# Kernel optimization log

Hardware: AMD Instinct MI355X
Metric: run time of the kernel (lower is better)

The kernel has to match this reference:

```python
import jax, jax.numpy as jnp
import numpy as np

B, T, H, DQK, DV = 2, 8192, 8, 128, 128
HID = H * DQK  # 1024
CHUNK = 64
EPS = 1e-5


def hedgehog(x, w, b):
    # torch Linear: y = x @ W.T + b, then softmax over cat([2y, -2y])
    y = x @ w.T + b
    return jax.nn.softmax(jnp.concatenate([2.0 * y, -2.0 * y], axis=-1), axis=-1)


def rmsnorm(x):
    return x * jax.lax.rsqrt(jnp.mean(x * x, axis=-1, keepdims=True) + EPS)


def chunk_linear_attn(q, k, v):
    # q, k: [B, T, H, Dk]; v: [B, T, H, Dv]  (head_first=False)
    scale = q.shape[-1] ** -0.5
    q = q * scale
    Bq, Tq, Hq, Dk = q.shape
    Dv = v.shape[-1]
    nc = Tq // CHUNK

    def to_chunks(t):
        # [B, T, H, D] -> [nc, B, H, C, D]
        return t.reshape(Bq, nc, CHUNK, Hq, -1).transpose(1, 0, 3, 2, 4)

    qc, kc, vc = to_chunks(q), to_chunks(k), to_chunks(v)
    mask = jnp.tril(jnp.ones((CHUNK, CHUNK), dtype=bool))

    def step(S, qkv):
        qi, ki, vi = qkv  # [B, H, C, D]
        attn = jnp.einsum('bhcd,bhed->bhce', qi, ki)      # intra-chunk scores
        attn = jnp.where(mask, attn, 0.0)                 # causal within chunk
        o = jnp.einsum('bhce,bhev->bhcv', attn, vi) \
            + jnp.einsum('bhcd,bhdv->bhcv', qi, S)        # inter-chunk via state
        S = S + jnp.einsum('bhcd,bhcv->bhdv', ki, vi)
        return S, o

    S0 = jnp.zeros((Bq, Hq, Dk, Dv), q.dtype)
    _, oc = jax.lax.scan(step, S0, (qc, kc, vc))          # oc: [nc, B, H, C, Dv]
    return oc.transpose(1, 0, 3, 2, 4).reshape(Bq, Tq, Hq, Dv)


def setup_inputs() -> dict:
    key = jax.random.key(0)
    ks = jax.random.split(key, 9)
    gain = 2.0 ** (-2.5)

    def xavier(k, shape):
        bound = gain * np.sqrt(6.0 / (shape[0] + shape[1]))
        return jax.random.uniform(k, shape, jnp.float32, -bound, bound)

    return {
        'x': jax.random.normal(ks[0], (B, T, HID), jnp.float32),
        'Wq': xavier(ks[1], (HID, HID)),
        'Wk': xavier(ks[2], (HID, HID)),
        'Wv': xavier(ks[3], (HID, HID)),
        'Wo': xavier(ks[4], (HID, HID)),
        # self.apply xavier-inits the hedgehog Linear layers too (no _is_hf_initialized flag)
        'fmq_w': xavier(ks[5], (DQK, DQK)),
        'fmq_b': jnp.zeros((DQK,), jnp.float32),
        'fmk_w': xavier(ks[6], (DQK, DQK)),
        'fmk_b': jnp.zeros((DQK,), jnp.float32),
    }


def reference(x, Wq, Wk, Wv, Wo, fmq_w, fmq_b, fmk_w, fmk_b):
    q = (x @ Wq.T).reshape(B, T, H, DQK)
    k = (x @ Wk.T).reshape(B, T, H, DQK)
    v = (x @ Wv.T).reshape(B, T, H, DV)
    q = hedgehog(q, fmq_w, fmq_b)   # [B, T, H, 2*DQK]
    k = hedgehog(k, fmk_w, fmk_b)   # [B, T, H, 2*DQK]
    o = chunk_linear_attn(q, k, v)  # [B, T, H, DV]
    o = rmsnorm(o.reshape(B, T, H * DV))
    return o @ Wo.T
```

## Files before the change

### kernel.cpp

```cpp
#include <hip/hip_runtime.h>
#include <stdint.h>

typedef unsigned short u16;
typedef __bf16 bf16x8 __attribute__((ext_vector_type(8)));
typedef float f32x4 __attribute__((ext_vector_type(4)));
typedef float f32x16 __attribute__((ext_vector_type(16)));

__device__ __forceinline__ u16 f2b(float f) {
  union { float f; unsigned u; } v; v.f = f;
  unsigned r = v.u + 0x7fffu + ((v.u >> 16) & 1u);
  return (u16)(r >> 16);
}
__device__ __forceinline__ float b2f(u16 b) {
  union { unsigned u; float f; } v; v.u = ((unsigned)b) << 16;
  return v.f;
}

__device__ __forceinline__ int swz64(int b) {
  return b ^ (((((b >> 6) & 3) ^ ((b >> 8) & 1))) << 4);
}

__global__ __launch_bounds__(256) void cast_bf16(const float* __restrict__ in,
                                                 u16* __restrict__ out, int n4) {
  int i = blockIdx.x * 256 + threadIdx.x;
  if (i >= n4) return;
  float4 f = ((const float4*)in)[i];
  ushort4 r = make_ushort4(f2b(f.x), f2b(f.y), f2b(f.z), f2b(f.w));
  ((ushort4*)out)[i] = r;
}

__global__ __launch_bounds__(256) void fold_w(const float* __restrict__ W,
                                              const float* __restrict__ fmw,
                                              u16* __restrict__ out) {
  int hj = blockIdx.x;
  int h = hj >> 7, j = hj & 127;
  int i0 = threadIdx.x * 4;
  float a0 = 0.f, a1 = 0.f, a2 = 0.f, a3 = 0.f;
  const float* Wh = W + (size_t)(h * 128) * 1024 + i0;
  const float* fw = fmw + j * 128;
  for (int d = 0; d < 128; ++d) {
    float wv = fw[d];
    const float* wr = Wh + (size_t)d * 1024;
    a0 += wv * wr[0]; a1 += wv * wr[1]; a2 += wv * wr[2]; a3 += wv * wr[3];
  }
  ushort4 r = make_ushort4(f2b(a0), f2b(a1), f2b(a2), f2b(a3));
  ((ushort4*)(out + (size_t)hj * 1024))[threadIdx.x] = r;
}

__global__ __launch_bounds__(512, 2) void gemm256(const u16* __restrict__ A,
                                                  const u16* __restrict__ B,
                                                  u16* __restrict__ C,
                                                  int M, int N, int K, int LNT) {
  __shared__ u16 lds[65536];
  const int tid = threadIdx.x, w = tid >> 6, lane = tid & 63;
  int g = blockIdx.x;
  int wg = (g & 7) * ((int)gridDim.x >> 3) + (g >> 3);
  const int nt = wg & ((1 << LNT) - 1), mt = wg >> LNT;
  const int m0 = mt << 8, n0 = nt << 8;
  const int wm = w >> 2, wn = w & 3;
  const int fm = lane & 15, fkb = (lane >> 4) << 4;

  int so0 = w * 1024 + lane * 16;
  int so1 = so0 + 8192;
  const int p0s = swz64(so0), p1s = swz64(so1);
  const size_t ga0 = (size_t)(p0s >> 6) * K + ((p0s & 63) >> 1);
  const size_t ga1 = (size_t)(p1s >> 6) * K + ((p1s & 63) >> 1);
  so0 >>= 1; so1 >>= 1;
#define STAGE(g0, slot)                                                               \
  do {                                                                                \
    __builtin_amdgcn_global_load_lds(                                                 \
        (const __attribute__((address_space(1))) unsigned int*)((g0) + ga0),          \
        (__attribute__((address_space(3))) unsigned int*)((slot) + so0), 16, 0, 0);   \
    __builtin_amdgcn_global_load_lds(                                                 \
        (const __attribute__((address_space(1))) unsigned int*)((g0) + ga1),          \
        (__attribute__((address_space(3))) unsigned int*)((slot) + so1), 16, 0, 0);   \
  } while (0)

  int aoff[2][4], boff[4];
#pragma unroll
  for (int mh = 0; mh < 2; ++mh)
#pragma unroll
    for (int mi = 0; mi < 4; ++mi)
      aoff[mh][mi] = swz64((wm * 128 + mh * 64 + mi * 16 + fm) * 64 + fkb) >> 1;
#pragma unroll
  for (int ni = 0; ni < 4; ++ni)
    boff[ni] = swz64((wn * 64 + ni * 16 + fm) * 64 + fkb) >> 1;

  const u16* Ag = A + (size_t)m0 * K;
  const u16* Bg = B + (size_t)n0 * K;
  const int NT = K >> 6;
  f32x4 acc[8][4] = {};

  STAGE(Ag, lds);
  STAGE(Bg, lds + 32768);
  STAGE(Ag + 32, lds + 8192);
  STAGE(Bg + 32, lds + 32768 + 8192);
  STAGE(Ag + 64, lds + 16384);
  STAGE(Bg + 64, lds + 32768 + 16384);
  asm volatile("s_waitcnt vmcnt(4)" ::: "memory");
  __builtin_amdgcn_s_barrier();

  for (int t = 0; t < NT; ++t) {
    const int buf = t & 1, nb = buf ^ 1;
    const u16* As0 = lds + buf * 16384;
    const u16* As1 = As0 + 8192;
    const u16* Bs0 = lds + 32768 + buf * 16384;
    const u16* Bs1 = Bs0 + 8192;
    bf16x8 a[4], bfr[4];

#pragma unroll
    for (int mi = 0; mi < 4; ++mi) a[mi] = *(const bf16x8*)(As0 + aoff[0][mi]);
#pragma unroll
    for (int ni = 0; ni < 4; ++ni) bfr[ni] = *(const bf16x8*)(Bs0 + boff[ni]);
    if (t + 1 < NT) STAGE(Ag + (t + 1) * 64 + 32, lds + nb * 16384 + 8192);
    __builtin_amdgcn_s_barrier();
    asm volatile("s_waitcnt lgkmcnt(0)" ::: "memory");
    __builtin_amdgcn_sched_barrier(0);
    __builtin_amdgcn_s_setprio(1);
#pragma unroll
    for (int mi = 0; mi < 4; ++mi)
#pragma unroll
      for (int ni = 0; ni < 4; ++ni)
        acc[mi][ni] = __builtin_amdgcn_mfma_f32_16x16x32_bf16(a[mi], bfr[ni], acc[mi][ni], 0, 0, 0);
    __builtin_amdgcn_s_setprio(0);
    __builtin_amdgcn_s_barrier();

#pragma unroll
    for (int mi = 0; mi < 4; ++mi) a[mi] = *(const bf16x8*)(As0 + aoff[1][mi]);
    if (t + 1 < NT) STAGE(Bg + (t + 1) * 64 + 32, lds + 32768 + nb * 16384 + 8192);
    __builtin_amdgcn_s_barrier();
    asm volatile("s_waitcnt lgkmcnt(0)" ::: "memory");
    __builtin_amdgcn_sched_barrier(0);
    __builtin_amdgcn_s_setprio(1);
#pragma unroll
    for (int mi = 0; mi < 4; ++mi)
#pragma unroll
      for (int ni = 0; ni < 4; ++ni)
        acc[4 + mi][ni] =
            __builtin_amdgcn_mfma_f32_16x16x32_bf16(a[mi], bfr[ni], acc[4 + mi][ni], 0, 0, 0);
    __builtin_amdgcn_s_setprio(0);
    __builtin_amdgcn_s_barrier();

#pragma unroll
    for (int mi = 0; mi < 4; ++mi) a[mi] = *(const bf16x8*)(As1 + aoff[0][mi]);
#pragma unroll
    for (int ni = 0; ni < 4; ++ni) bfr[ni] = *(const bf16x8*)(Bs1 + boff[ni]);
    if (t + 2 < NT) STAGE(Ag + (t + 2) * 64, lds + buf * 16384);
    __builtin_amdgcn_s_barrier();
    asm volatile("s_waitcnt lgkmcnt(0)" ::: "memory");
    __builtin_amdgcn_sched_barrier(0);
    __builtin_amdgcn_s_setprio(1);
#pragma unroll
    for (int mi = 0; mi < 4; ++mi)
#pragma unroll
      for (int ni = 0; ni < 4; ++ni)
        acc[mi][ni] = __builtin_amdgcn_mfma_f32_16x16x32_bf16(a[mi], bfr[ni], acc[mi][ni], 0, 0, 0);
    __builtin_amdgcn_s_setprio(0);
    __builtin_amdgcn_s_barrier();

#pragma unroll
    for (int mi = 0; mi < 4; ++mi) a[mi] = *(const bf16x8*)(As1 + aoff[1][mi]);
    if (t + 2 < NT) STAGE(Bg + (t + 2) * 64, lds + 32768 + buf * 16384);
    __builtin_amdgcn_s_barrier();
    asm volatile("s_waitcnt lgkmcnt(0)" ::: "memory");
    __builtin_amdgcn_sched_barrier(0);
    __builtin_amdgcn_s_setprio(1);
#pragma unroll
    for (int mi = 0; mi < 4; ++mi)
#pragma unroll
      for (int ni = 0; ni < 4; ++ni)
        acc[4 + mi][ni] =
            __builtin_amdgcn_mfma_f32_16x16x32_bf16(a[mi], bfr[ni], acc[4 + mi][ni], 0, 0, 0);
    __builtin_amdgcn_s_setprio(0);
    if (t < NT - 2)
      asm volatile("s_waitcnt vmcnt(4)" ::: "memory");
    else
      asm volatile("s_waitcnt vmcnt(0)" ::: "memory");
    __builtin_amdgcn_s_barrier();
  }
#undef STAGE

  u16* Cs = lds;
  const int cr = (lane >> 4) << 2, cc = lane & 15;
#pragma unroll
  for (int am = 0; am < 8; ++am)
#pragma unroll
    for (int ni = 0; ni < 4; ++ni)
#pragma unroll
      for (int r = 0; r < 4; ++r)
        Cs[(wm * 128 + (am >> 2) * 64 + (am & 3) * 16 + cr + r) * 256 + wn * 64 + ni * 16 + cc] =
            f2b(acc[am][ni][r]);
  __syncthreads();
#pragma unroll
  for (int pass = 0; pass < 16; ++pass) {
    int row = pass * 16 + (tid >> 5);
    int colb = (tid & 31) << 4;
    *(uint4*)((char*)(C + (size_t)(m0 + row) * N + n0) + colb) =
        *(const uint4*)((const char*)(Cs + row * 256) + colb);
  }
}

template <int OUT_BF16>
__global__ __launch_bounds__(256) void gemm_bt(const u16* __restrict__ A,
                                               const u16* __restrict__ B,
                                               void* __restrict__ Cv,
                                               int M, int N, int K, int SWZ, int LNT) {
  __shared__ u16 smem[16384];
  u16* As = smem;
  u16* Bs = smem + 8192;
  const int tid = threadIdx.x;
  int g = blockIdx.y * gridDim.x + blockIdx.x;
  int xcd = g & 7, local = g >> 3;
  int mt, nt;
  if (SWZ == 0) {
    mt = xcd * ((int)gridDim.y >> 3) + (local >> LNT);
    nt = local & ((1 << LNT) - 1);
  } else {
    nt = xcd * ((int)gridDim.x >> 3) + (local >> 3);
    mt = local & 7;
  }
  const int m0 = mt * 128, n0 = nt * 128;
  const int wave = tid >> 6, lane = tid & 63;
  const int wm = (wave >> 1) << 6, wn = (wave & 1) << 6;
  f32x4 acc[4][4] = {};
  const int srow = tid >> 3;
  const int scol = (tid & 7) << 3;
  const u16* Ab = A + (size_t)(m0 + srow) * K + scol;
  const u16* Bb = B + (size_t)(n0 + srow) * K + scol;
  u16* Asp = As + srow * 64 + scol;
  u16* Bsp = Bs + srow * 64 + scol;
  const int fm = lane & 15;
  const int fk = (lane >> 4) << 3;
  for (int kt = 0; kt < K; kt += 64) {
#pragma unroll
    for (int i = 0; i < 4; ++i) {
      __builtin_amdgcn_global_load_lds(
          (__attribute__((address_space(1))) unsigned int*)(Ab + (size_t)i * 32 * K + kt),
          (__attribute__((address_space(3))) unsigned int*)(Asp + i * 32 * 64), 16, 0, 0);
      __builtin_amdgcn_global_load_lds(
          (__attribute__((address_space(1))) unsigned int*)(Bb + (size_t)i * 32 * K + kt),
          (__attribute__((address_space(3))) unsigned int*)(Bsp + i * 32 * 64), 16, 0, 0);
    }
    __syncthreads();
#pragma unroll
    for (int kb = 0; kb < 2; ++kb) {
      bf16x8 af[4], bfr[4];
#pragma unroll
      for (int i = 0; i < 4; ++i)
        af[i] = *(const bf16x8*)(As + (wm + i * 16 + fm) * 64 + kb * 32 + fk);
#pragma unroll
      for (int j = 0; j < 4; ++j)
        bfr[j] = *(const bf16x8*)(Bs + (wn + j * 16 + fm) * 64 + kb * 32 + fk);
#pragma unroll
      for (int i = 0; i < 4; ++i)
#pragma unroll
        for (int j = 0; j < 4; ++j)
          acc[i][j] = __builtin_amdgcn_mfma_f32_16x16x32_bf16(af[i], bfr[j], acc[i][j], 0, 0, 0);
    }
    __syncthreads();
  }
  const int cr = (lane >> 4) << 2;
  const int cc = lane & 15;
  if (OUT_BF16) {
    u16* Cs = smem;
#pragma unroll
    for (int i = 0; i < 4; ++i)
#pragma unroll
      for (int j = 0; j < 4; ++j)
#pragma unroll
        for (int r = 0; r < 4; ++r)
          Cs[(wm + i * 16 + cr + r) * 128 + wn + j * 16 + cc] = f2b(acc[i][j][r]);
    __syncthreads();
    u16* Cg = (u16*)Cv;
#pragma unroll
    for (int i = 0; i < 8; ++i) {
      int row = (i >> 1) * 32 + (tid >> 3);
      int col = ((i & 1) * 8 + (tid & 7)) * 8;
      *(uint4*)(Cg + (size_t)(m0 + row) * N + n0 + col) = *(const uint4*)(Cs + row * 128 + col);
    }
  } else {
    float* Csf = (float*)smem;
    float* Cg = (float*)Cv;
#pragma unroll
    for (int hh = 0; hh < 2; ++hh) {
      __syncthreads();
      if ((wm >> 6) == hh) {
#pragma unroll
        for (int i = 0; i < 4; ++i)
#pragma unroll
          for (int j = 0; j < 4; ++j)
#pragma unroll
            for (int r = 0; r < 4; ++r)
              Csf[(i * 16 + cr + r) * 128 + wn + j * 16 + cc] = acc[i][j][r];
      }
      __syncthreads();
#pragma unroll
      for (int i = 0; i < 8; ++i) {
        int row = (i >> 1) * 16 + (tid >> 4);
        int col = ((i & 1) * 16 + (tid & 15)) * 4;
        *(float4*)(Cg + (size_t)(m0 + hh * 64 + row) * N + n0 + col) =
            *(const float4*)(Csf + row * 128 + col);
      }
    }
  }
}

__global__ __launch_bounds__(256) void hedgehog_sm(const u16* __restrict__ y,
                                                   const float* __restrict__ bias,
                                                   u16* __restrict__ phi, float scale,
                                                   int colbase) {
  int wave = threadIdx.x >> 6, lane = threadIdx.x & 63;
  int rh = blockIdx.x * 4 + wave;
  const u16* yr = y + (size_t)(rh >> 3) * 2048 + colbase + (rh & 7) * 128;
  float a1 = 2.f * (b2f(yr[lane]) + bias[lane]);
  float a2 = 2.f * (b2f(yr[lane + 64]) + bias[lane + 64]);
  float mx = fmaxf(fabsf(a1), fabsf(a2));
#pragma unroll
  for (int off = 32; off; off >>= 1) mx = fmaxf(mx, __shfl_xor(mx, off, 64));
  float e1 = __expf(a1 - mx), e2 = __expf(a2 - mx);
  float n1 = __expf(-a1 - mx), n2 = __expf(-a2 - mx);
  float s = e1 + e2 + n1 + n2;
#pragma unroll
  for (int off = 32; off; off >>= 1) s += __shfl_xor(s, off, 64);
  float inv = scale / s;
  u16* pr = phi + (size_t)rh * 256;
  pr[lane] = f2b(e1 * inv);
  pr[lane + 64] = f2b(e2 * inv);
  pr[lane + 128] = f2b(n1 * inv);
  pr[lane + 192] = f2b(n2 * inv);
}

__global__ __launch_bounds__(256, 1) void attn_intra_kv2(const u16* __restrict__ phi_q,
                                                         const u16* __restrict__ phi_k,
                                                         const u16* __restrict__ vt,
                                                         float* __restrict__ o,
                                                         u16* __restrict__ kv) {
  __shared__ u16 lds[18432];
  u16* At = lds;
  u16* Kt = lds;
  int g = blockIdx.x;
  int n = g & 63, h = g >> 6;
  int t0 = n * 128;
  const u16* qg = phi_q + ((size_t)t0 * 8 + h) * 256;
  const u16* kg = phi_k + ((size_t)t0 * 8 + h) * 256;
  const u16* vg = vt + (size_t)(h * 128) * 8192 + t0;
  int tid = threadIdx.x, lane = tid & 63, w = tid >> 6;
  const int fr = lane & 31, fg = (lane >> 5) << 3;
  const int rbase = (lane >> 5) << 2;
  const int mw = (w >> 1) << 6;
  const int nw = (w & 1) << 6;

  f32x16 accS[2][2] = {};
#pragma unroll
  for (int ks = 0; ks < 16; ++ks) {
    bf16x8 a[2], b[2];
#pragma unroll
    for (int i = 0; i < 2; ++i)
      a[i] = *(const bf16x8*)(qg + (size_t)(mw + i * 32 + fr) * 2048 + ks * 16 + fg);
#pragma unroll
    for (int j = 0; j < 2; ++j)
      b[j] = *(const bf16x8*)(kg + (size_t)(nw + j * 32 + fr) * 2048 + ks * 16 + fg);
#pragma unroll
    for (int i = 0; i < 2; ++i)
#pragma unroll
      for (int j = 0; j < 2; ++j)
        accS[i][j] = __builtin_amdgcn_mfma_f32_32x32x16_bf16(a[i], b[j], accS[i][j], 0, 0, 0);
  }
#pragma unroll
  for (int i = 0; i < 2; ++i)
#pragma unroll
    for (int j = 0; j < 2; ++j) {
      int col = nw + j * 32 + (lane & 31);
#pragma unroll
      for (int r = 0; r < 16; ++r) {
        int row = mw + i * 32 + (r & 3) + ((r >> 2) << 3) + rbase;
        At[row * 136 + col] = f2b(col <= row ? accS[i][j][r] : 0.f);
      }
    }
  __syncthreads();
  f32x16 accO[2][2] = {};
#pragma unroll
  for (int ks = 0; ks < 8; ++ks) {
    bf16x8 a[2], b[2];
#pragma unroll
    for (int i = 0; i < 2; ++i)
      a[i] = *(const bf16x8*)(At + (mw + i * 32 + fr) * 136 + ks * 16 + fg);
#pragma unroll
    for (int j = 0; j < 2; ++j)
      b[j] = *(const bf16x8*)(vg + (size_t)(nw + j * 32 + fr) * 8192 + ks * 16 + fg);
#pragma unroll
    for (int i = 0; i < 2; ++i)
#pragma unroll
      for (int j = 0; j < 2; ++j)
        accO[i][j] = __builtin_amdgcn_mfma_f32_32x32x16_bf16(a[i], b[j], accO[i][j], 0, 0, 0);
  }
  {
    float* og = o + ((size_t)t0 * 8 + h) * 128;
#pragma unroll
    for (int i = 0; i < 2; ++i)
#pragma unroll
      for (int j = 0; j < 2; ++j) {
        int vc = nw + j * 32 + (lane & 31);
#pragma unroll
        for (int r = 0; r < 16; ++r) {
          int row = mw + i * 32 + (r & 3) + ((r >> 2) << 3) + rbase;
          og[(size_t)row * 1024 + vc] = accO[i][j][r];
        }
      }
  }
  __syncthreads();

  const int nd = w << 6;
  f32x16 accKV[4][2] = {};
#pragma unroll
  for (int hb = 0; hb < 2; ++hb) {
    {
      int r4 = (tid & 15) << 2;
      int d0 = (tid >> 4) << 4;
      u16 tmp[4][16];
#pragma unroll
      for (int r = 0; r < 4; ++r) {
        const u16* src = kg + (size_t)(hb * 64 + r4 + r) * 2048 + d0;
        *(uint4*)(tmp[r]) = *(const uint4*)src;
        *(uint4*)(tmp[r] + 8) = *(const uint4*)(src + 8);
      }
#pragma unroll
      for (int jj = 0; jj < 16; ++jj) {
        ushort4 pk = make_ushort4(tmp[0][jj], tmp[1][jj], tmp[2][jj], tmp[3][jj]);
        *(ushort4*)(Kt + (d0 + jj) * 72 + r4) = pk;
      }
    }
    __syncthreads();
#pragma unroll
    for (int ks = 0; ks < 4; ++ks) {
      bf16x8 a[4], b[2];
#pragma unroll
      for (int mi = 0; mi < 4; ++mi)
        a[mi] = *(const bf16x8*)(vg + (size_t)(mi * 32 + fr) * 8192 + hb * 64 + ks * 16 + fg);
#pragma unroll
      for (int nj = 0; nj < 2; ++nj)
        b[nj] = *(const bf16x8*)(Kt + (nd + nj * 32 + fr) * 72 + ks * 16 + fg);
#pragma unroll
      for (int mi = 0; mi < 4; ++mi)
#pragma unroll
        for (int nj = 0; nj < 2; ++nj)
          accKV[mi][nj] =
              __builtin_amdgcn_mfma_f32_32x32x16_bf16(a[mi], b[nj], accKV[mi][nj], 0, 0, 0);
    }
    __syncthreads();
  }
  {
    u16* kvg = kv + (size_t)g * 32768;
#pragma unroll
    for (int mi = 0; mi < 4; ++mi)
#pragma unroll
      for (int nj = 0; nj < 2; ++nj) {
        f32x16 acc = accKV[mi][nj];
        int d = nd + nj * 32 + (lane & 31);
#pragma unroll
        for (int r = 0; r < 16; ++r) {
          int vc = mi * 32 + (r & 3) + ((r >> 2) << 3) + rbase;
          kvg[(size_t)vc * 256 + d] = f2b(acc[r]);
        }
      }
  }
}

__global__ __launch_bounds__(256) void kv_scan2(u16* __restrict__ kv) {
  int idx = blockIdx.x * 256 + threadIdx.x;
  int h = idx >> 13;
  int e4 = idx & 8191;
  u16* p = kv + (size_t)h * 2097152 + (size_t)e4 * 4;
  float run[4] = {};
  for (int nn = 0; nn < 64; ++nn) {
    uint2 raw = *(const uint2*)p;
    u16* rv = (u16*)&raw;
    uint2 outw;
    u16* ov = (u16*)&outw;
#pragma unroll
    for (int i = 0; i < 4; ++i) {
      float v = b2f(rv[i]);
      ov[i] = f2b(run[i]);
      run[i] += v;
    }
    *(uint2*)p = outw;
    p += 32768;
  }
}

__global__ __launch_bounds__(256, 1) void attn_inter2(const u16* __restrict__ phi_q,
                                                      const u16* __restrict__ kv,
                                                      float* __restrict__ o) {
  int g = blockIdx.x;
  int n = g & 63, h = g >> 6;
  int t0 = n * 128;
  const u16* qg = phi_q + ((size_t)t0 * 8 + h) * 256;
  const u16* sg = kv + (size_t)g * 32768;
  int tid = threadIdx.x, lane = tid & 63, w = tid >> 6;
  const int fr = lane & 31, fg = (lane >> 5) << 3;
  const int rbase = (lane >> 5) << 2;
  const int mw = (w >> 1) << 6;
  const int nw = (w & 1) << 6;
  f32x16 acc[2][2] = {};
#pragma unroll
  for (int ks = 0; ks < 16; ++ks) {
    bf16x8 a[2], b[2];
#pragma unroll
    for (int i = 0; i < 2; ++i)
      a[i] = *(const bf16x8*)(qg + (size_t)(mw + i * 32 + fr) * 2048 + ks * 16 + fg);
#pragma unroll
    for (int j = 0; j < 2; ++j)
      b[j] = *(const bf16x8*)(sg + (size_t)(nw + j * 32 + fr) * 256 + ks * 16 + fg);
#pragma unroll
    for (int i = 0; i < 2; ++i)
#pragma unroll
      for (int j = 0; j < 2; ++j)
        acc[i][j] = __builtin_amdgcn_mfma_f32_32x32x16_bf16(a[i], b[j], acc[i][j], 0, 0, 0);
  }
  float* og = o + ((size_t)t0 * 8 + h) * 128;
#pragma unroll
  for (int i = 0; i < 2; ++i)
#pragma unroll
    for (int j = 0; j < 2; ++j) {
      int vc = nw + j * 32 + (lane & 31);
#pragma unroll
      for (int r = 0; r < 16; ++r) {
        int row = mw + i * 32 + (r & 3) + ((r >> 2) << 3) + rbase;
        og[(size_t)row * 1024 + vc] += acc[i][j][r];
      }
    }
}

__global__ __launch_bounds__(256) void rmsnorm_k(const float* __restrict__ o,
                                                 u16* __restrict__ on) {
  __shared__ float red[4];
  int row = blockIdx.x;
  const float* orow = o + (size_t)row * 1024;
  int tid = threadIdx.x;
  float4 v = ((const float4*)orow)[tid];
  float ss = v.x * v.x + v.y * v.y + v.z * v.z + v.w * v.w;
#pragma unroll
  for (int off = 32; off; off >>= 1) ss += __shfl_xor(ss, off, 64);
  if ((tid & 63) == 0) red[tid >> 6] = ss;
  __syncthreads();
  float tot = red[0] + red[1] + red[2] + red[3];
  float rms = rsqrtf(tot * (1.f / 1024.f) + 1e-5f);
  ushort4 r = make_ushort4(f2b(v.x * rms), f2b(v.y * rms), f2b(v.z * rms), f2b(v.w * rms));
  ((ushort4*)(on + (size_t)row * 1024))[tid] = r;
}

extern "C" void kernel_launch(void* const* d_in, const int* in_sizes, int n_in,
                              void* d_out, int out_size, void* d_ws, size_t ws_size,
                              hipStream_t stream) {
  const float* x     = (const float*)d_in[0];
  const float* Wq    = (const float*)d_in[1];
  const float* Wk    = (const float*)d_in[2];
  const float* Wv    = (const float*)d_in[3];
  const float* Wo    = (const float*)d_in[4];
  const float* fmq_w = (const float*)d_in[5];
  const float* fmq_b = (const float*)d_in[6];
  const float* fmk_w = (const float*)d_in[7];
  const float* fmk_b = (const float*)d_in[8];

  char* ws = (char*)d_ws;
  u16*   kvb  = (u16*)(ws + 0);
  u16*   xb   = (u16*)(ws + 0);
  u16*   yb   = (u16*)(ws + 16777216);
  u16*   onb  = (u16*)(ws + 50331648);
  u16*   phiq = (u16*)(ws + 67108864);
  u16*   phik = (u16*)(ws + 100663296);
  u16*   vtb  = (u16*)(ws + 134217728);
  float* obuf = (float*)(ws + 150994944);
  u16*   wqkc = (u16*)(ws + 184549376);
  u16*   wvb  = (u16*)(ws + 188743680);
  u16*   wob  = (u16*)(ws + 190840832);

  cast_bf16<<<1024, 256, 0, stream>>>(Wv, wvb, 262144);
  cast_bf16<<<1024, 256, 0, stream>>>(Wo, wob, 262144);
  fold_w<<<1024, 256, 0, stream>>>(Wq, fmq_w, wqkc);
  fold_w<<<1024, 256, 0, stream>>>(Wk, fmk_w, wqkc + 1048576);

  for (int b = 0; b < 2; ++b) {
    const float* xsrc = x + (size_t)b * 8388608;
    float* osrc = (float*)d_out + (size_t)b * 8388608;
    cast_bf16<<<8192, 256, 0, stream>>>(xsrc, xb, 2097152);
    gemm256<<<256, 512, 0, stream>>>(xb, wqkc, yb, 8192, 2048, 1024, 3);
    hedgehog_sm<<<16384, 256, 0, stream>>>(yb, fmq_b, phiq, 0.0625f, 0);
    hedgehog_sm<<<16384, 256, 0, stream>>>(yb, fmk_b, phik, 1.0f, 1024);
    gemm_bt<1><<<dim3(64, 8), 256, 0, stream>>>(wvb, xb, vtb, 1024, 8192, 1024, 1, 0);
    attn_intra_kv2<<<512, 256, 0, stream>>>(phiq, phik, vtb, obuf, kvb);
    kv_scan2<<<256, 256, 0, stream>>>(kvb);
    attn_inter2<<<512, 256, 0, stream>>>(phiq, kvb, obuf);
    rmsnorm_k<<<8192, 256, 0, stream>>>(obuf, onb);
    gemm_bt<0><<<dim3(8, 64), 256, 0, stream>>>(onb, wob, osrc, 8192, 1024, 1024, 0, 3);
  }
}
```

Before: 666.2 us.

## Stage K, Q and V tiles in swizzled LDS via async global-to-LDS loads in attention kernel

The intra-chunk attention kernel now copies the whole phi_k tile, the V^T tile and each half of phi_q into 128 KB of LDS using global_load_lds, with an XOR swizzle. The QK^T, AV and K^T V MFMA loops then read operands from LDS instead of issuing strided global loads directly into registers. The A and K-transpose scratch buffers are re-laid out with swizzles in place of padding, and __syncthreads is replaced by explicit waitcnt plus barrier. This is meant to cut redundant global traffic and uncoalesced loads, at the cost of far more LDS per block and forcing one block per CU.

After: 642.1 us. -3.6%, faster.

```diff
diff --git a/kernel.cpp b/kernel.cpp
--- a/kernel.cpp
+++ b/kernel.cpp
@@ -19,6 +19,8 @@
 __device__ __forceinline__ int swz64(int b) {
   return b ^ (((((b >> 6) & 3) ^ ((b >> 8) & 1))) << 4);
 }
+
+#define SB0() __builtin_amdgcn_sched_barrier(0)
 
 __global__ __launch_bounds__(256) void cast_bf16(const float* __restrict__ in,
                                                  u16* __restrict__ out, int n4) {
@@ -115,7 +117,7 @@
     if (t + 1 < NT) STAGE(Ag + (t + 1) * 64 + 32, lds + nb * 16384 + 8192);
     __builtin_amdgcn_s_barrier();
     asm volatile("s_waitcnt lgkmcnt(0)" ::: "memory");
-    __builtin_amdgcn_sched_barrier(0);
+    SB0();
     __builtin_amdgcn_s_setprio(1);
 #pragma unroll
     for (int mi = 0; mi < 4; ++mi)
@@ -130,7 +132,7 @@
     if (t + 1 < NT) STAGE(Bg + (t + 1) * 64 + 32, lds + 32768 + nb * 16384 + 8192);
     __builtin_amdgcn_s_barrier();
     asm volatile("s_waitcnt lgkmcnt(0)" ::: "memory");
-    __builtin_amdgcn_sched_barrier(0);
+    SB0();
     __builtin_amdgcn_s_setprio(1);
 #pragma unroll
     for (int mi = 0; mi < 4; ++mi)
@@ -148,7 +150,7 @@
     if (t + 2 < NT) STAGE(Ag + (t + 2) * 64, lds + buf * 16384);
     __builtin_amdgcn_s_barrier();
     asm volatile("s_waitcnt lgkmcnt(0)" ::: "memory");
-    __builtin_amdgcn_sched_barrier(0);
+    SB0();
     __builtin_amdgcn_s_setprio(1);
 #pragma unroll
     for (int mi = 0; mi < 4; ++mi)
@@ -163,7 +165,7 @@
     if (t + 2 < NT) STAGE(Bg + (t + 2) * 64, lds + 32768 + buf * 16384);
     __builtin_amdgcn_s_barrier();
     asm volatile("s_waitcnt lgkmcnt(0)" ::: "memory");
-    __builtin_amdgcn_sched_barrier(0);
+    SB0();
     __builtin_amdgcn_s_setprio(1);
 #pragma unroll
     for (int mi = 0; mi < 4; ++mi)
@@ -330,14 +332,17 @@
   pr[lane + 192] = f2b(n2 * inv);
 }
 
-__global__ __launch_bounds__(256, 1) void attn_intra_kv2(const u16* __restrict__ phi_q,
-                                                         const u16* __restrict__ phi_k,
-                                                         const u16* __restrict__ vt,
-                                                         float* __restrict__ o,
-                                                         u16* __restrict__ kv) {
-  __shared__ u16 lds[18432];
-  u16* At = lds;
-  u16* Kt = lds;
+__global__ __launch_bounds__(256, 1) void attn_fused(const u16* __restrict__ phi_q,
+                                                     const u16* __restrict__ phi_k,
+                                                     const u16* __restrict__ vt,
+                                                     float* __restrict__ o,
+                                                     u16* __restrict__ kv) {
+  __shared__ u16 lds[65536];
+  u16* Ks = lds;
+  u16* Vs = lds + 32768;
+  u16* Qh = lds + 49152;
+  u16* At = lds + 49152;
+  u16* Kt = lds + 49152;
   int g = blockIdx.x;
   int n = g & 63, h = g >> 6;
   int t0 = n * 128;
@@ -350,22 +355,78 @@
   const int mw = (w >> 1) << 6;
   const int nw = (w & 1) << 6;
 
+  const int c8 = (tid & 31) << 3;
+  const int rkq = tid >> 5;
+  const int cv = (tid & 15) << 3;
+  const int rv = tid >> 4;
+#pragma unroll
+  for (int i = 0; i < 16; ++i) {
+    int row = i * 8 + rkq;
+    int cs = c8 ^ ((row & 15) << 3);
+    __builtin_amdgcn_global_load_lds(
+        (const __attribute__((address_space(1))) unsigned int*)(kg + (size_t)row * 2048 + cs),
+        (__attribute__((address_space(3))) unsigned int*)(Ks + i * 2048 + tid * 8), 16, 0, 0);
+  }
+#pragma unroll
+  for (int i = 0; i < 8; ++i) {
+    int row = i * 16 + rv;
+    int cs = cv ^ ((row & 15) << 3);
+    __builtin_amdgcn_global_load_lds(
+        (const __attribute__((address_space(1))) unsigned int*)(qg + (size_t)row * 2048 + cs),
+        (__attribute__((address_space(3))) unsigned int*)(Qh + i * 2048 + tid * 8), 16, 0, 0);
+  }
+#pragma unroll
+  for (int i = 0; i < 8; ++i) {
+    int row = i * 16 + rv;
+    int cs = cv ^ ((row & 15) << 3);
+    __builtin_amdgcn_global_load_lds(
+        (const __attribute__((address_space(1))) unsigned int*)(vg + (size_t)row * 8192 + cs),
+        (__attribute__((address_space(3))) unsigned int*)(Vs + i * 2048 + tid * 8), 16, 0, 0);
+  }
+  asm volatile("s_waitcnt vmcnt(8)" ::: "memory");
+  SB0(); __builtin_amdgcn_s_barrier(); SB0();
+
   f32x16 accS[2][2] = {};
-#pragma unroll
-  for (int ks = 0; ks < 16; ++ks) {
-    bf16x8 a[2], b[2];
-#pragma unroll
-    for (int i = 0; i < 2; ++i)
-      a[i] = *(const bf16x8*)(qg + (size_t)(mw + i * 32 + fr) * 2048 + ks * 16 + fg);
-#pragma unroll
-    for (int j = 0; j < 2; ++j)
-      b[j] = *(const bf16x8*)(kg + (size_t)(nw + j * 32 + fr) * 2048 + ks * 16 + fg);
-#pragma unroll
-    for (int i = 0; i < 2; ++i)
-#pragma unroll
-      for (int j = 0; j < 2; ++j)
-        accS[i][j] = __builtin_amdgcn_mfma_f32_32x32x16_bf16(a[i], b[j], accS[i][j], 0, 0, 0);
-  }
+  const int ra0 = mw + fr, ra1 = mw + 32 + fr;
+  const int rb0 = nw + fr, rb1 = nw + 32 + fr;
+  const int xa0 = (ra0 & 15) << 3, xa1 = (ra1 & 15) << 3;
+  const int xb0 = (rb0 & 15) << 3, xb1 = (rb1 & 15) << 3;
+#pragma unroll
+  for (int pass = 0; pass < 2; ++pass) {
+    const int kb = pass << 7;
+#pragma unroll
+    for (int ks = 0; ks < 8; ++ks) {
+      int col = ks * 16 + fg;
+      bf16x8 a[2], b[2];
+      a[0] = *(const bf16x8*)(Qh + ra0 * 128 + (col ^ xa0));
+      a[1] = *(const bf16x8*)(Qh + ra1 * 128 + (col ^ xa1));
+      b[0] = *(const bf16x8*)(Ks + rb0 * 256 + ((kb + col) ^ xb0));
+      b[1] = *(const bf16x8*)(Ks + rb1 * 256 + ((kb + col) ^ xb1));
+#pragma unroll
+      for (int i = 0; i < 2; ++i)
+#pragma unroll
+        for (int j = 0; j < 2; ++j)
+          accS[i][j] = __builtin_amdgcn_mfma_f32_32x32x16_bf16(a[i], b[j], accS[i][j], 0, 0, 0);
+    }
+    if (pass == 0) {
+      asm volatile("s_waitcnt lgkmcnt(0)" ::: "memory");
+      SB0(); __builtin_amdgcn_s_barrier(); SB0();
+#pragma unroll
+      for (int i = 0; i < 8; ++i) {
+        int row = i * 16 + rv;
+        int cs = cv ^ ((row & 15) << 3);
+        __builtin_amdgcn_global_load_lds(
+            (const __attribute__((address_space(1))) unsigned int*)(qg + (size_t)row * 2048 +
+                                                                    128 + cs),
+            (__attribute__((address_space(3))) unsigned int*)(Qh + i * 2048 + tid * 8), 16, 0, 0);
+      }
+      asm volatile("s_waitcnt vmcnt(0)" ::: "memory");
+      SB0(); __builtin_amdgcn_s_barrier(); SB0();
+    }
+  }
+  asm volatile("s_waitcnt lgkmcnt(0)" ::: "memory");
+  SB0(); __builtin_amdgcn_s_barrier(); SB0();
+
 #pragma unroll
   for (int i = 0; i < 2; ++i)
 #pragma unroll
@@ -374,25 +435,29 @@
 #pragma unroll
       for (int r = 0; r < 16; ++r) {
         int row = mw + i * 32 + (r & 3) + ((r >> 2) << 3) + rbase;
-        At[row * 136 + col] = f2b(col <= row ? accS[i][j][r] : 0.f);
-      }
-    }
-  __syncthreads();
+        At[row * 128 + (col ^ ((row & 15) << 3))] = f2b(col <= row ? accS[i][j][r] : 0.f);
+      }
+    }
+  asm volatile("s_waitcnt lgkmcnt(0)" ::: "memory");
+  SB0(); __builtin_amdgcn_s_barrier(); SB0();
+
   f32x16 accO[2][2] = {};
-#pragma unroll
-  for (int ks = 0; ks < 8; ++ks) {
-    bf16x8 a[2], b[2];
-#pragma unroll
-    for (int i = 0; i < 2; ++i)
-      a[i] = *(const bf16x8*)(At + (mw + i * 32 + fr) * 136 + ks * 16 + fg);
-#pragma unroll
-    for (int j = 0; j < 2; ++j)
-      b[j] = *(const bf16x8*)(vg + (size_t)(nw + j * 32 + fr) * 8192 + ks * 16 + fg);
-#pragma unroll
-    for (int i = 0; i < 2; ++i)
-#pragma unroll
-      for (int j = 0; j < 2; ++j)
-        accO[i][j] = __builtin_amdgcn_mfma_f32_32x32x16_bf16(a[i], b[j], accO[i][j], 0, 0, 0);
+  {
+    const int xv0 = (rb0 & 15) << 3, xv1 = (rb1 & 15) << 3;
+#pragma unroll
+    for (int ks = 0; ks < 8; ++ks) {
+      int col = ks * 16 + fg;
+      bf16x8 a[2], b[2];
+      a[0] = *(const bf16x8*)(At + ra0 * 128 + (col ^ xa0));
+      a[1] = *(const bf16x8*)(At + ra1 * 128 + (col ^ xa1));
+      b[0] = *(const bf16x8*)(Vs + rb0 * 128 + (col ^ xv0));
+      b[1] = *(const bf16x8*)(Vs + rb1 * 128 + (col ^ xv1));
+#pragma unroll
+      for (int i = 0; i < 2; ++i)
+#pragma unroll
+        for (int j = 0; j < 2; ++j)
+          accO[i][j] = __builtin_amdgcn_mfma_f32_32x32x16_bf16(a[i], b[j], accO[i][j], 0, 0, 0);
+    }
   }
   {
     float* og = o + ((size_t)t0 * 8 + h) * 128;
@@ -408,7 +473,8 @@
         }
       }
   }
-  __syncthreads();
+  asm volatile("s_waitcnt lgkmcnt(0)" ::: "memory");
+  SB0(); __builtin_amdgcn_s_barrier(); SB0();
 
   const int nd = w << 6;
   f32x16 accKV[4][2] = {};
@@ -420,26 +486,34 @@
       u16 tmp[4][16];
 #pragma unroll
       for (int r = 0; r < 4; ++r) {
-        const u16* src = kg + (size_t)(hb * 64 + r4 + r) * 2048 + d0;
-        *(uint4*)(tmp[r]) = *(const uint4*)src;
-        *(uint4*)(tmp[r] + 8) = *(const uint4*)(src + 8);
+        int row = hb * 64 + r4 + r;
+        int xm = (row & 15) << 3;
+        const u16* src = Ks + row * 256;
+        *(uint4*)(tmp[r]) = *(const uint4*)(src + (d0 ^ xm));
+        *(uint4*)(tmp[r] + 8) = *(const uint4*)(src + ((d0 + 8) ^ xm));
       }
 #pragma unroll
       for (int jj = 0; jj < 16; ++jj) {
         ushort4 pk = make_ushort4(tmp[0][jj], tmp[1][jj], tmp[2][jj], tmp[3][jj]);
-        *(ushort4*)(Kt + (d0 + jj) * 72 + r4) = pk;
-      }
-    }
-    __syncthreads();
+        *(ushort4*)(Kt + (d0 + jj) * 64 + (r4 ^ ((jj & 7) << 3))) = pk;
+      }
+    }
+    asm volatile("s_waitcnt lgkmcnt(0)" ::: "memory");
+    SB0(); __builtin_amdgcn_s_barrier(); SB0();
 #pragma unroll
     for (int ks = 0; ks < 4; ++ks) {
       bf16x8 a[4], b[2];
 #pragma unroll
-      for (int mi = 0; mi < 4; ++mi)
-        a[mi] = *(const bf16x8*)(vg + (size_t)(mi * 32 + fr) * 8192 + hb * 64 + ks * 16 + fg);
-#pragma unroll
-      for (int nj = 0; nj < 2; ++nj)
-        b[nj] = *(const bf16x8*)(Kt + (nd + nj * 32 + fr) * 72 + ks * 16 + fg);
+      for (int mi = 0; mi < 4; ++mi) {
+        int rvv = mi * 32 + fr;
+        a[mi] = *(const bf16x8*)(Vs + rvv * 128 +
+                                 ((hb * 64 + ks * 16 + fg) ^ ((rvv & 15) << 3)));
+      }
+#pragma unroll
+      for (int nj = 0; nj < 2; ++nj) {
+        int rk = nd + nj * 32 + fr;
+        b[nj] = *(const bf16x8*)(Kt + rk * 64 + ((ks * 16 + fg) ^ ((rk & 7) << 3)));
+      }
 #pragma unroll
       for (int mi = 0; mi < 4; ++mi)
 #pragma unroll
@@ -447,7 +521,8 @@
           accKV[mi][nj] =
               __builtin_amdgcn_mfma_f32_32x32x16_bf16(a[mi], b[nj], accKV[mi][nj], 0, 0, 0);
     }
-    __syncthreads();
+    asm volatile("s_waitcnt lgkmcnt(0)" ::: "memory");
+    SB0(); __builtin_amdgcn_s_barrier(); SB0();
   }
   {
     u16* kvg = kv + (size_t)g * 32768;
@@ -588,7 +663,7 @@
     hedgehog_sm<<<16384, 256, 0, stream>>>(yb, fmq_b, phiq, 0.0625f, 0);
     hedgehog_sm<<<16384, 256, 0, stream>>>(yb, fmk_b, phik, 1.0f, 1024);
     gemm_bt<1><<<dim3(64, 8), 256, 0, stream>>>(wvb, xb, vtb, 1024, 8192, 1024, 1, 0);
-    attn_intra_kv2<<<512, 256, 0, stream>>>(phiq, phik, vtb, obuf, kvb);
+    attn_fused<<<512, 256, 0, stream>>>(phiq, phik, vtb, obuf, kvb);
     kv_scan2<<<256, 256, 0, stream>>>(kvb);
     attn_inter2<<<512, 256, 0, stream>>>(phiq, kvb, obuf);
     rmsnorm_k<<<8192, 256, 0, stream>>>(obuf, onb);
```

## Halve attention chunk size to 64 tokens, doubling block count

Applied to the files above, without the earlier changes.

The intra-chunk, KV-state, scan and inter-chunk attention kernels now work on 64-token chunks instead of 128. This halves the quadratic intra-chunk score and output work and launches 1024 blocks instead of 512, for better occupancy across the compute units. In exchange, twice as many 128x128 KV states are written, scanned over 128 steps and read back, which doubles that memory traffic. The KV buffer must also be twice as large.

Result: no change. 656.0 us (-1.5%).

```diff
diff --git a/kernel.cpp b/kernel.cpp
--- a/kernel.cpp
+++ b/kernel.cpp
@@ -19,6 +19,8 @@
 __device__ __forceinline__ int swz64(int b) {
   return b ^ (((((b >> 6) & 3) ^ ((b >> 8) & 1))) << 4);
 }
+
+#define SB0() __builtin_amdgcn_sched_barrier(0)
 
 __global__ __launch_bounds__(256) void cast_bf16(const float* __restrict__ in,
                                                  u16* __restrict__ out, int n4) {
@@ -115,7 +117,7 @@
     if (t + 1 < NT) STAGE(Ag + (t + 1) * 64 + 32, lds + nb * 16384 + 8192);
     __builtin_amdgcn_s_barrier();
     asm volatile("s_waitcnt lgkmcnt(0)" ::: "memory");
-    __builtin_amdgcn_sched_barrier(0);
+    SB0();
     __builtin_amdgcn_s_setprio(1);
 #pragma unroll
     for (int mi = 0; mi < 4; ++mi)
@@ -130,7 +132,7 @@
     if (t + 1 < NT) STAGE(Bg + (t + 1) * 64 + 32, lds + 32768 + nb * 16384 + 8192);
     __builtin_amdgcn_s_barrier();
     asm volatile("s_waitcnt lgkmcnt(0)" ::: "memory");
-    __builtin_amdgcn_sched_barrier(0);
+    SB0();
     __builtin_amdgcn_s_setprio(1);
 #pragma unroll
     for (int mi = 0; mi < 4; ++mi)
@@ -148,7 +150,7 @@
     if (t + 2 < NT) STAGE(Ag + (t + 2) * 64, lds + buf * 16384);
     __builtin_amdgcn_s_barrier();
     asm volatile("s_waitcnt lgkmcnt(0)" ::: "memory");
-    __builtin_amdgcn_sched_barrier(0);
+    SB0();
     __builtin_amdgcn_s_setprio(1);
 #pragma unroll
     for (int mi = 0; mi < 4; ++mi)
@@ -163,7 +165,7 @@
     if (t + 2 < NT) STAGE(Bg + (t + 2) * 64, lds + 32768 + buf * 16384);
     __builtin_amdgcn_s_barrier();
     asm volatile("s_waitcnt lgkmcnt(0)" ::: "memory");
-    __builtin_amdgcn_sched_barrier(0);
+    SB0();
     __builtin_amdgcn_s_setprio(1);
 #pragma unroll
     for (int mi = 0; mi < 4; ++mi)
@@ -330,124 +332,101 @@
   pr[lane + 192] = f2b(n2 * inv);
 }
 
-__global__ __launch_bounds__(256, 1) void attn_intra_kv2(const u16* __restrict__ phi_q,
-                                                         const u16* __restrict__ phi_k,
-                                                         const u16* __restrict__ vt,
-                                                         float* __restrict__ o,
-                                                         u16* __restrict__ kv) {
+__global__ __launch_bounds__(256, 1) void attn_intra64(const u16* __restrict__ phi_q,
+                                                       const u16* __restrict__ phi_k,
+                                                       const u16* __restrict__ vt,
+                                                       float* __restrict__ o,
+                                                       u16* __restrict__ kv) {
   __shared__ u16 lds[18432];
   u16* At = lds;
   u16* Kt = lds;
   int g = blockIdx.x;
-  int n = g & 63, h = g >> 6;
-  int t0 = n * 128;
+  int n = g & 127, h = g >> 7;
+  int t0 = n * 64;
   const u16* qg = phi_q + ((size_t)t0 * 8 + h) * 256;
   const u16* kg = phi_k + ((size_t)t0 * 8 + h) * 256;
   const u16* vg = vt + (size_t)(h * 128) * 8192 + t0;
   int tid = threadIdx.x, lane = tid & 63, w = tid >> 6;
   const int fr = lane & 31, fg = (lane >> 5) << 3;
   const int rbase = (lane >> 5) << 2;
-  const int mw = (w >> 1) << 6;
-  const int nw = (w & 1) << 6;
-
-  f32x16 accS[2][2] = {};
+  const int mw = (w >> 1) << 5;
+  const int nw = (w & 1) << 5;
+  const int nv = (w & 1) << 6;
+
+  f32x16 accS = {};
 #pragma unroll
   for (int ks = 0; ks < 16; ++ks) {
-    bf16x8 a[2], b[2];
-#pragma unroll
-    for (int i = 0; i < 2; ++i)
-      a[i] = *(const bf16x8*)(qg + (size_t)(mw + i * 32 + fr) * 2048 + ks * 16 + fg);
-#pragma unroll
-    for (int j = 0; j < 2; ++j)
-      b[j] = *(const bf16x8*)(kg + (size_t)(nw + j * 32 + fr) * 2048 + ks * 16 + fg);
-#pragma unroll
-    for (int i = 0; i < 2; ++i)
-#pragma unroll
-      for (int j = 0; j < 2; ++j)
-        accS[i][j] = __builtin_amdgcn_mfma_f32_32x32x16_bf16(a[i], b[j], accS[i][j], 0, 0, 0);
-  }
-#pragma unroll
-  for (int i = 0; i < 2; ++i)
-#pragma unroll
-    for (int j = 0; j < 2; ++j) {
-      int col = nw + j * 32 + (lane & 31);
-#pragma unroll
-      for (int r = 0; r < 16; ++r) {
-        int row = mw + i * 32 + (r & 3) + ((r >> 2) << 3) + rbase;
-        At[row * 136 + col] = f2b(col <= row ? accS[i][j][r] : 0.f);
-      }
-    }
+    bf16x8 a = *(const bf16x8*)(qg + (size_t)(mw + fr) * 2048 + ks * 16 + fg);
+    bf16x8 b = *(const bf16x8*)(kg + (size_t)(nw + fr) * 2048 + ks * 16 + fg);
+    accS = __builtin_amdgcn_mfma_f32_32x32x16_bf16(a, b, accS, 0, 0, 0);
+  }
+  {
+    int col = nw + (lane & 31);
+#pragma unroll
+    for (int r = 0; r < 16; ++r) {
+      int row = mw + (r & 3) + ((r >> 2) << 3) + rbase;
+      At[row * 136 + col] = f2b(col <= row ? accS[r] : 0.f);
+    }
+  }
   __syncthreads();
-  f32x16 accO[2][2] = {};
-#pragma unroll
-  for (int ks = 0; ks < 8; ++ks) {
-    bf16x8 a[2], b[2];
-#pragma unroll
-    for (int i = 0; i < 2; ++i)
-      a[i] = *(const bf16x8*)(At + (mw + i * 32 + fr) * 136 + ks * 16 + fg);
-#pragma unroll
-    for (int j = 0; j < 2; ++j)
-      b[j] = *(const bf16x8*)(vg + (size_t)(nw + j * 32 + fr) * 8192 + ks * 16 + fg);
-#pragma unroll
-    for (int i = 0; i < 2; ++i)
-#pragma unroll
-      for (int j = 0; j < 2; ++j)
-        accO[i][j] = __builtin_amdgcn_mfma_f32_32x32x16_bf16(a[i], b[j], accO[i][j], 0, 0, 0);
+  f32x16 accO[2] = {};
+#pragma unroll
+  for (int ks = 0; ks < 4; ++ks) {
+    bf16x8 a = *(const bf16x8*)(At + (mw + fr) * 136 + ks * 16 + fg);
+#pragma unroll
+    for (int nj = 0; nj < 2; ++nj) {
+      bf16x8 b = *(const bf16x8*)(vg + (size_t)(nv + nj * 32 + fr) * 8192 + ks * 16 + fg);
+      accO[nj] = __builtin_amdgcn_mfma_f32_32x32x16_bf16(a, b, accO[nj], 0, 0, 0);
+    }
   }
   {
     float* og = o + ((size_t)t0 * 8 + h) * 128;
 #pragma unroll
-    for (int i = 0; i < 2; ++i)
-#pragma unroll
-      for (int j = 0; j < 2; ++j) {
-        int vc = nw + j * 32 + (lane & 31);
-#pragma unroll
-        for (int r = 0; r < 16; ++r) {
-          int row = mw + i * 32 + (r & 3) + ((r >> 2) << 3) + rbase;
-          og[(size_t)row * 1024 + vc] = accO[i][j][r];
-        }
+    for (int nj = 0; nj < 2; ++nj) {
+      int vc = nv + nj * 32 + (lane & 31);
+#pragma unroll
+      for (int r = 0; r < 16; ++r) {
+        int row = mw + (r & 3) + ((r >> 2) << 3) + rbase;
+        og[(size_t)row * 1024 + vc] = accO[nj][r];
       }
+    }
   }
   __syncthreads();
 
+  {
+    int r4 = (tid & 15) << 2;
+    int d0 = (tid >> 4) << 4;
+    u16 tmp[4][16];
+#pragma unroll
+    for (int r = 0; r < 4; ++r) {
+      const u16* src = kg + (size_t)(r4 + r) * 2048 + d0;
+      *(uint4*)(tmp[r]) = *(const uint4*)src;
+      *(uint4*)(tmp[r] + 8) = *(const uint4*)(src + 8);
+    }
+#pragma unroll
+    for (int jj = 0; jj < 16; ++jj) {
+      ushort4 pk = make_ushort4(tmp[0][jj], tmp[1][jj], tmp[2][jj], tmp[3][jj]);
+      *(ushort4*)(Kt + (d0 + jj) * 72 + r4) = pk;
+    }
+  }
+  __syncthreads();
   const int nd = w << 6;
   f32x16 accKV[4][2] = {};
 #pragma unroll
-  for (int hb = 0; hb < 2; ++hb) {
-    {
-      int r4 = (tid & 15) << 2;
-      int d0 = (tid >> 4) << 4;
-      u16 tmp[4][16];
-#pragma unroll
-      for (int r = 0; r < 4; ++r) {
-        const u16* src = kg + (size_t)(hb * 64 + r4 + r) * 2048 + d0;
-        *(uint4*)(tmp[r]) = *(const uint4*)src;
-        *(uint4*)(tmp[r] + 8) = *(const uint4*)(src + 8);
-      }
-#pragma unroll
-      for (int jj = 0; jj < 16; ++jj) {
-        ushort4 pk = make_ushort4(tmp[0][jj], tmp[1][jj], tmp[2][jj], tmp[3][jj]);
-        *(ushort4*)(Kt + (d0 + jj) * 72 + r4) = pk;
-      }
-    }
-    __syncthreads();
-#pragma unroll
-    for (int ks = 0; ks < 4; ++ks) {
-      bf16x8 a[4], b[2];
-#pragma unroll
-      for (int mi = 0; mi < 4; ++mi)
-        a[mi] = *(const bf16x8*)(vg + (size_t)(mi * 32 + fr) * 8192 + hb * 64 + ks * 16 + fg);
+  for (int ks = 0; ks < 4; ++ks) {
+    bf16x8 a[4], b[2];
+#pragma unroll
+    for (int mi = 0; mi < 4; ++mi)
+      a[mi] = *(const bf16x8*)(vg + (size_t)(mi * 32 + fr) * 8192 + ks * 16 + fg);
+#pragma unroll
+    for (int nj = 0; nj < 2; ++nj)
+      b[nj] = *(const bf16x8*)(Kt + (nd + nj * 32 + fr) * 72 + ks * 16 + fg);
+#pragma unroll
+    for (int mi = 0; mi < 4; ++mi)
 #pragma unroll
       for (int nj = 0; nj < 2; ++nj)
-        b[nj] = *(const bf16x8*)(Kt + (nd + nj * 32 + fr) * 72 + ks * 16 + fg);
-#pragma unroll
-      for (int mi = 0; mi < 4; ++mi)
-#pragma unroll
-        for (int nj = 0; nj < 2; ++nj)
-          accKV[mi][nj] =
-              __builtin_amdgcn_mfma_f32_32x32x16_bf16(a[mi], b[nj], accKV[mi][nj], 0, 0, 0);
-    }
-    __syncthreads();
+        accKV[mi][nj] =
+            __builtin_amdgcn_mfma_f32_32x32x16_bf16(a[mi], b[nj], accKV[mi][nj], 0, 0, 0);
   }
   {
     u16* kvg = kv + (size_t)g * 32768;
@@ -466,13 +445,14 @@
   }
 }
 
-__global__ __launch_bounds__(256) void kv_scan2(u16* __restrict__ kv) {
+__global__ __launch_bounds__(256) void kv_scan64(u16* __restrict__ kv) {
   int idx = blockIdx.x * 256 + threadIdx.x;
   int h = idx >> 13;
   int e4 = idx & 8191;
-  u16* p = kv + (size_t)h * 2097152 + (size_t)e4 * 4;
+  u16* p = kv + (size_t)h * 4194304 + (size_t)e4 * 4;
   float run[4] = {};
-  for (int nn = 0; nn < 64; ++nn) {
+#pragma unroll 4
+  for (int nn = 0; nn < 128; ++nn) {
     uint2 raw = *(const uint2*)p;
     u16* rv = (u16*)&raw;
     uint2 outw;
@@ -488,47 +468,39 @@
   }
 }
 
-__global__ __launch_bounds__(256, 1) void attn_inter2(const u16* __restrict__ phi_q,
-                                                      const u16* __restrict__ kv,
-                                                      float* __restrict__ o) {
+__global__ __launch_bounds__(256, 1) void attn_inter64(const u16* __restrict__ phi_q,
+                                                       const u16* __restrict__ kv,
+                                                       float* __restrict__ o) {
   int g = blockIdx.x;
-  int n = g & 63, h = g >> 6;
-  int t0 = n * 128;
+  int n = g & 127, h = g >> 7;
+  int t0 = n * 64;
   const u16* qg = phi_q + ((size_t)t0 * 8 + h) * 256;
   const u16* sg = kv + (size_t)g * 32768;
   int tid = threadIdx.x, lane = tid & 63, w = tid >> 6;
   const int fr = lane & 31, fg = (lane >> 5) << 3;
   const int rbase = (lane >> 5) << 2;
-  const int mw = (w >> 1) << 6;
-  const int nw = (w & 1) << 6;
-  f32x16 acc[2][2] = {};
+  const int mw = (w >> 1) << 5;
+  const int nv = (w & 1) << 6;
+  f32x16 acc[2] = {};
 #pragma unroll
   for (int ks = 0; ks < 16; ++ks) {
-    bf16x8 a[2], b[2];
-#pragma unroll
-    for (int i = 0; i < 2; ++i)
-      a[i] = *(const bf16x8*)(qg + (size_t)(mw + i * 32 + fr) * 2048 + ks * 16 + fg);
-#pragma unroll
-    for (int j = 0; j < 2; ++j)
-      b[j] = *(const bf16x8*)(sg + (size_t)(nw + j * 32 + fr) * 256 + ks * 16 + fg);
-#pragma unroll
-    for (int i = 0; i < 2; ++i)
-#pragma unroll
-      for (int j = 0; j < 2; ++j)
-        acc[i][j] = __builtin_amdgcn_mfma_f32_32x32x16_bf16(a[i], b[j], acc[i][j], 0, 0, 0);
+    bf16x8 a = *(const bf16x8*)(qg + (size_t)(mw + fr) * 2048 + ks * 16 + fg);
+#pragma unroll
+    for (int nj = 0; nj < 2; ++nj) {
+      bf16x8 b = *(const bf16x8*)(sg + (size_t)(nv + nj * 32 + fr) * 256 + ks * 16 + fg);
+      acc[nj] = __builtin_amdgcn_mfma_f32_32x32x16_bf16(a, b, acc[nj], 0, 0, 0);
+    }
   }
   float* og = o + ((size_t)t0 * 8 + h) * 128;
 #pragma unroll
-  for (int i = 0; i < 2; ++i)
-#pragma unroll
-    for (int j = 0; j < 2; ++j) {
-      int vc = nw + j * 32 + (lane & 31);
-#pragma unroll
-      for (int r = 0; r < 16; ++r) {
-        int row = mw + i * 32 + (r & 3) + ((r >> 2) << 3) + rbase;
-        og[(size_t)row * 1024 + vc] += acc[i][j][r];
-      }
-    }
+  for (int nj = 0; nj < 2; ++nj) {
+    int vc = nv + nj * 32 + (lane & 31);
+#pragma unroll
+    for (int r = 0; r < 16; ++r) {
+      int row = mw + (r & 3) + ((r >> 2) << 3) + rbase;
+      og[(size_t)row * 1024 + vc] += acc[nj][r];
+    }
+  }
 }
 
 __global__ __launch_bounds__(256) void rmsnorm_k(const float* __restrict__ o,
@@ -588,9 +560,9 @@
     hedgehog_sm<<<16384, 256, 0, stream>>>(yb, fmq_b, phiq, 0.0625f, 0);
     hedgehog_sm<<<16384, 256, 0, stream>>>(yb, fmk_b, phik, 1.0f, 1024);
     gemm_bt<1><<<dim3(64, 8), 256, 0, stream>>>(wvb, xb, vtb, 1024, 8192, 1024, 1, 0);
-    attn_intra_kv2<<<512, 256, 0, stream>>>(phiq, phik, vtb, obuf, kvb);
-    kv_scan2<<<256, 256, 0, stream>>>(kvb);
-    attn_inter2<<<512, 256, 0, stream>>>(phiq, kvb, obuf);
+    attn_intra64<<<1024, 256, 0, stream>>>(phiq, phik, vtb, obuf, kvb);
+    kv_scan64<<<256, 256, 0, stream>>>(kvb);
+    attn_inter64<<<1024, 256, 0, stream>>>(phiq, kvb, obuf);
     rmsnorm_k<<<8192, 256, 0, stream>>>(obuf, onb);
     gemm_bt<0><<<dim3(8, 64), 256, 0, stream>>>(onb, wob, osrc, 8192, 1024, 1024, 0, 3);
   }
```
